# Kernel optimization log

Measured on AMD Instinct MI355X. Metric: run time of the kernel, lower is better.

Reference implementation:

```python
import jax, jax.numpy as jnp
import numpy as np

BN_EPS = 1e-5
NEG_SLOPE = 0.2

def _bn(x, g, b, m, v):
    # inference-mode BatchNorm1d over the channel (last) axis
    return (x - m) * jax.lax.rsqrt(v + BN_EPS) * g + b

def _lrelu(x):
    return jnp.where(x >= 0, x, NEG_SLOPE * x)

def setup_inputs() -> dict:
    key = jax.random.key(0)
    ks = jax.random.split(key, 24)
    B, N, K, Cr, Cin, Cnb, Cout = 2, 65536, 16, 10, 64, 64, 128
    Ccat = Cin + Cnb
    return {
        'xyz': jax.random.normal(ks[0], (B, N, 3), jnp.float32),
        'feature': jax.random.normal(ks[1], (B, N, Cin), jnp.float32),
        'raw_neighbors_feature': jax.random.normal(ks[2], (B, N, K, Cr), jnp.float32),
        'neighbors_idx': jax.random.randint(ks[3], (B, N, K), 0, N, jnp.int32),
        'W_nb': jax.random.normal(ks[4], (Cr, Cnb), jnp.float32) * 0.3,
        'b_nb': jax.random.normal(ks[5], (Cnb,), jnp.float32),
        'g_nb': jax.random.uniform(ks[6], (Cnb,), jnp.float32),
        'be_nb': jax.random.normal(ks[7], (Cnb,), jnp.float32),
        'm_nb': jax.random.normal(ks[8], (Cnb,), jnp.float32),
        'v_nb': jax.random.uniform(ks[9], (Cnb,), jnp.float32),
        'W_attn': jax.random.normal(ks[10], (Ccat, Ccat), jnp.float32) * 0.09,
        'W_out': jax.random.normal(ks[11], (Ccat, Cout), jnp.float32) * 0.09,
        'b_out': jax.random.normal(ks[12], (Cout,), jnp.float32),
        'g_out': jax.random.uniform(ks[13], (Cout,), jnp.float32),
        'be_out': jax.random.normal(ks[14], (Cout,), jnp.float32),
        'm_out': jax.random.normal(ks[15], (Cout,), jnp.float32),
        'v_out': jax.random.uniform(ks[16], (Cout,), jnp.float32),
        'W_sc': jax.random.normal(ks[17], (Cin, Cout), jnp.float32) * 0.12,
        'b_sc': jax.random.normal(ks[18], (Cout,), jnp.float32),
        'g_sc': jax.random.uniform(ks[19], (Cout,), jnp.float32),
        'be_sc': jax.random.normal(ks[20], (Cout,), jnp.float32),
        'm_sc': jax.random.normal(ks[21], (Cout,), jnp.float32),
        'v_sc': jax.random.uniform(ks[22], (Cout,), jnp.float32),
    }

def reference(xyz, feature, raw_neighbors_feature, neighbors_idx,
              W_nb, b_nb, g_nb, be_nb, m_nb, v_nb,
              W_attn,
              W_out, b_out, g_out, be_out, m_out, v_out,
              W_sc, b_sc, g_sc, be_sc, m_sc, v_sc):
    # mlp_neighbor_fea: Linear -> BN1d -> leaky_relu(0.2) over raw neighbor features
    nb = _lrelu(_bn(jnp.einsum('bnkc,cd->bnkd', raw_neighbors_feature, W_nb) + b_nb,
                    g_nb, be_nb, m_nb, v_nb))              # [B,N,K,Cnb]
    # index_points: gather per-point neighbor features [B,N,K,Cin]
    gathered = jax.vmap(lambda f, i: f[i])(feature, neighbors_idx)
    fea = jnp.concatenate([gathered, nb], axis=-1)          # [B,N,K,Ccat]
    # attn pooling: softmax over neighbor axis K of a bias-free linear
    attn = jax.nn.softmax(jnp.einsum('bnkc,cd->bnkd', fea, W_attn), axis=2)
    pooled = jnp.sum(attn * fea, axis=2)                    # [B,N,Ccat]
    out_branch = _bn(pooled @ W_out + b_out, g_out, be_out, m_out, v_out)
    sc_branch = _bn(feature @ W_sc + b_sc, g_sc, be_sc, m_sc, v_sc)
    return _lrelu(sc_branch + out_branch)                   # [B,N,Cout]
```

## Files before the change

kernel.cpp:

```cpp
#include <hip/hip_runtime.h>


#define KNB   16
#define CR    10
#define CIN   64
#define CCAT  128
#define COUT  128
#define NPTS  131072
#define EPS   1e-5f

#define WS_WB   0
#define WS_W3   32768
#define WS_WNB  81920
#define WS_B3   86016
#define WS_BNB  86528

typedef const float* fp;
typedef short bf16x8 __attribute__((ext_vector_type(8)));
typedef float f32x4  __attribute__((ext_vector_type(4)));

__device__ __forceinline__ unsigned short f2bf(float x) {
    unsigned int u = __float_as_uint(x);
    return (unsigned short)((u + 0x7FFFu + ((u >> 16) & 1u)) >> 16);
}
__device__ __forceinline__ unsigned int pack2(float a, float b) {
    return (unsigned int)f2bf(a) | ((unsigned int)f2bf(b) << 16);
}
__device__ __forceinline__ float bf2f(unsigned short h) {
    return __uint_as_float(((unsigned int)h) << 16);
}
__device__ __forceinline__ float lrelu(float x) { return fmaxf(x, 0.2f * x); }

__global__ __launch_bounds__(256) void lfa_prep(
    fp W_nb, fp b_nb, fp g_nb, fp be_nb, fp m_nb, fp v_nb,
    fp W_attn,
    fp W_out, fp b_out, fp g_out, fp be_out, fp m_out, fp v_out,
    fp W_sc,  fp b_sc,  fp g_sc,  fp be_sc,  fp m_sc,  fp v_sc,
    unsigned char* __restrict__ ws)
{
    const int t = blockIdx.x * 256 + threadIdx.x;
    if (t < 2048) {
        const int n0 = t >> 8, s = (t >> 6) & 3, ln = t & 63;
        const int n = (n0 << 4) + (ln & 15);
        unsigned int v[4];
        #pragma unroll
        for (int jj = 0; jj < 4; ++jj) {
            const int k = (s << 5) + ((ln >> 4) << 3) + jj * 2;
            v[jj] = pack2(W_attn[k * CCAT + n], W_attn[(k + 1) * CCAT + n]);
        }
        *(uint4*)(ws + WS_WB + t * 16) = make_uint4(v[0], v[1], v[2], v[3]);
    } else if (t < 5120) {
        const int e = t - 2048;
        const int t8 = e / 384, rem = e % 384, s = rem >> 6, ln = rem & 63;
        const int d = (t8 << 4) + (ln & 15);
        const float so = g_out[d] * rsqrtf(v_out[d] + EPS);
        const float ss = g_sc[d]  * rsqrtf(v_sc[d]  + EPS);
        unsigned int v[4];
        #pragma unroll
        for (int jj = 0; jj < 4; ++jj) {
            float a[2];
            #pragma unroll
            for (int h = 0; h < 2; ++h) {
                const int k = (s << 5) + ((ln >> 4) << 3) + jj * 2 + h;
                a[h] = (k < CCAT) ? W_out[k * COUT + d] * so
                                  : W_sc[(k - CCAT) * COUT + d] * ss;
            }
            v[jj] = pack2(a[0], a[1]);
        }
        *(uint4*)(ws + WS_W3 + e * 16) = make_uint4(v[0], v[1], v[2], v[3]);
    } else if (t < 5376) {
        const int e = t - 5120;
        const int n0 = e >> 6, ln = e & 63;
        const int n = (n0 << 4) + (ln & 15);
        const float sn = g_nb[n] * rsqrtf(v_nb[n] + EPS);
        unsigned int v[4];
        #pragma unroll
        for (int jj = 0; jj < 4; ++jj) {
            float a[2];
            #pragma unroll
            for (int h = 0; h < 2; ++h) {
                const int k = ((ln >> 4) << 3) + jj * 2 + h;
                a[h] = (k < CR) ? W_nb[k * 64 + n] * sn : 0.f;
            }
            v[jj] = pack2(a[0], a[1]);
        }
        *(uint4*)(ws + WS_WNB + e * 16) = make_uint4(v[0], v[1], v[2], v[3]);
    } else if (t < 5504) {
        const int d = t - 5376;
        const float so = g_out[d] * rsqrtf(v_out[d] + EPS);
        const float ss = g_sc[d]  * rsqrtf(v_sc[d]  + EPS);
        ((float*)(ws + WS_B3))[d] =
              (b_out[d] - m_out[d]) * so + be_out[d]
            + (b_sc[d]  - m_sc[d])  * ss + be_sc[d];
    } else if (t < 5568) {
        const int d = t - 5504;
        const float sn = g_nb[d] * rsqrtf(v_nb[d] + EPS);
        ((float*)(ws + WS_BNB))[d] = (b_nb[d] - m_nb[d]) * sn + be_nb[d];
    }
}

__global__ __launch_bounds__(256, 2) void lfa_main(
    fp feature, fp raw, const int* __restrict__ nidx,
    const unsigned char* __restrict__ ws, float* __restrict__ out)
{
    __shared__ __align__(16) unsigned short feaA[4][2][16][136];
    __shared__ __align__(16) unsigned short pooledA[4][16][200];

    const int tid  = threadIdx.x;
    const int w    = tid >> 6;
    const int lane = tid & 63;
    const int quad = lane >> 4;
    const int l15  = lane & 15;
    const int p0   = (blockIdx.x * 4 + w) * 16;
    const int b    = p0 >> 16;

    bf16x8 WB[8][4];
    #pragma unroll
    for (int n0 = 0; n0 < 8; ++n0)
        #pragma unroll
        for (int s = 0; s < 4; ++s)
            WB[n0][s] = *(const bf16x8*)(ws + WS_WB + (((n0 * 4 + s) * 64 + lane) << 4));

    float binb[4];
    #pragma unroll
    for (int j = 0; j < 4; ++j)
        binb[j] = ((const float*)(ws + WS_BNB))[j * 16 + l15];

    #pragma unroll 1
    for (int it = 0; it < 8; ++it) {
        const int pp0 = p0 + it * 2;

        int idxv = 0;
        if (lane < 32) idxv = nidx[pp0 * KNB + lane];

        if (lane < 32) {
            const int pt = lane >> 4, c4 = l15 * 4;
            const float4 cf = *(const float4*)&feature[(size_t)(pp0 + pt) * CIN + c4];
            uint2 pk; pk.x = pack2(cf.x, cf.y); pk.y = pack2(cf.z, cf.w);
            *(uint2*)&pooledA[w][it * 2 + pt][CCAT + c4] = pk;
        }

        #pragma unroll
        for (int pt = 0; pt < 2; ++pt) {
            const int p = pp0 + pt;

            float4 gv[4];
            #pragma unroll
            for (int i = 0; i < 4; ++i) {
                const int ni = __shfl(idxv, pt * 16 + i * 4 + quad, 64);
                gv[i] = *(const float4*)&feature[(size_t)((b << 16) + ni) * CIN + l15 * 4];
            }

            bf16x8 anb = {0, 0, 0, 0, 0, 0, 0, 0};
            {
                const float* rp = raw + (size_t)p * (KNB * CR) + l15 * CR;
                if (quad == 0) {
                    const float2 r0 = *(const float2*)(rp + 0);
                    const float2 r1 = *(const float2*)(rp + 2);
                    const float2 r2 = *(const float2*)(rp + 4);
                    const float2 r3 = *(const float2*)(rp + 6);
                    anb[0] = (short)f2bf(r0.x); anb[1] = (short)f2bf(r0.y);
                    anb[2] = (short)f2bf(r1.x); anb[3] = (short)f2bf(r1.y);
                    anb[4] = (short)f2bf(r2.x); anb[5] = (short)f2bf(r2.y);
                    anb[6] = (short)f2bf(r3.x); anb[7] = (short)f2bf(r3.y);
                } else if (quad == 1) {
                    const float2 r4 = *(const float2*)(rp + 8);
                    anb[0] = (short)f2bf(r4.x); anb[1] = (short)f2bf(r4.y);
                }
            }

            float nbC[4][4];
            #pragma unroll
            for (int n0 = 0; n0 < 4; ++n0) {
                const bf16x8 bw = *(const bf16x8*)(ws + WS_WNB + ((n0 * 64 + lane) << 4));
                f32x4 c = {0.f, 0.f, 0.f, 0.f};
                c = __builtin_amdgcn_mfma_f32_16x16x32_bf16(anb, bw, c, 0, 0, 0);
                #pragma unroll
                for (int r = 0; r < 4; ++r) {
                    const float x = lrelu(c[r] + binb[n0]);
                    nbC[n0][r] = x;
                    feaA[w][pt][quad * 4 + r][64 + n0 * 16 + l15] = f2bf(x);
                }
            }

            #pragma unroll
            for (int i = 0; i < 4; ++i) {
                uint2 pk; pk.x = pack2(gv[i].x, gv[i].y); pk.y = pack2(gv[i].z, gv[i].w);
                *(uint2*)&feaA[w][pt][i * 4 + quad][l15 * 4] = pk;
            }

            bf16x8 A[4];
            #pragma unroll
            for (int s = 0; s < 4; ++s)
                A[s] = *(const bf16x8*)&feaA[w][pt][l15][s * 32 + quad * 8];

            #pragma unroll
            for (int n0 = 0; n0 < 8; ++n0) {
                f32x4 c = {0.f, 0.f, 0.f, 0.f};
                #pragma unroll
                for (int s = 0; s < 4; ++s)
                    c = __builtin_amdgcn_mfma_f32_16x16x32_bf16(A[s], WB[n0][s], c, 0, 0, 0);
                const float e0 = __expf(c[0]), e1 = __expf(c[1]);
                const float e2 = __expf(c[2]), e3 = __expf(c[3]);
                float den = e0 + e1 + e2 + e3;
                float num;
                if (n0 < 4) {
                    num = e0 * bf2f(feaA[w][pt][quad * 4 + 0][n0 * 16 + l15])
                        + e1 * bf2f(feaA[w][pt][quad * 4 + 1][n0 * 16 + l15])
                        + e2 * bf2f(feaA[w][pt][quad * 4 + 2][n0 * 16 + l15])
                        + e3 * bf2f(feaA[w][pt][quad * 4 + 3][n0 * 16 + l15]);
                } else {
                    num = e0 * nbC[n0 - 4][0] + e1 * nbC[n0 - 4][1]
                        + e2 * nbC[n0 - 4][2] + e3 * nbC[n0 - 4][3];
                }
                num += __shfl_xor(num, 16, 64);
                den += __shfl_xor(den, 16, 64);
                num += __shfl_xor(num, 32, 64);
                den += __shfl_xor(den, 32, 64);
                const float pp = __fdividef(num, den);
                if (quad == 0)
                    pooledA[w][it * 2 + pt][n0 * 16 + l15] = f2bf(pp);
            }
        }
    }

    bf16x8 A3[6];
    #pragma unroll
    for (int s = 0; s < 6; ++s)
        A3[s] = *(const bf16x8*)&pooledA[w][l15][s * 32 + quad * 8];
    #pragma unroll
    for (int t = 0; t < 8; ++t) {
        f32x4 c = {0.f, 0.f, 0.f, 0.f};
        #pragma unroll
        for (int s = 0; s < 6; ++s) {
            const bf16x8 bw = *(const bf16x8*)(ws + WS_W3 + (((t * 6 + s) * 64 + lane) << 4));
            c = __builtin_amdgcn_mfma_f32_16x16x32_bf16(A3[s], bw, c, 0, 0, 0);
        }
        const float bz = ((const float*)(ws + WS_B3))[t * 16 + l15];
        #pragma unroll
        for (int r = 0; r < 4; ++r)
            out[(size_t)(p0 + quad * 4 + r) * COUT + t * 16 + l15] = lrelu(c[r] + bz);
    }
}

extern "C" void kernel_launch(void* const* d_in, const int* in_sizes, int n_in,
                              void* d_out, int out_size, void* d_ws, size_t ws_size,
                              hipStream_t stream)
{
    fp feature = (fp)d_in[1];
    fp raw     = (fp)d_in[2];
    const int* nidx = (const int*)d_in[3];
    fp W_nb = (fp)d_in[4],  b_nb = (fp)d_in[5],  g_nb = (fp)d_in[6];
    fp be_nb = (fp)d_in[7], m_nb = (fp)d_in[8],  v_nb = (fp)d_in[9];
    fp W_attn = (fp)d_in[10];
    fp W_out = (fp)d_in[11], b_out = (fp)d_in[12], g_out = (fp)d_in[13];
    fp be_out = (fp)d_in[14], m_out = (fp)d_in[15], v_out = (fp)d_in[16];
    fp W_sc = (fp)d_in[17], b_sc = (fp)d_in[18], g_sc = (fp)d_in[19];
    fp be_sc = (fp)d_in[20], m_sc = (fp)d_in[21], v_sc = (fp)d_in[22];

    hipLaunchKernelGGL(lfa_prep, dim3(22), dim3(256), 0, stream,
                       W_nb, b_nb, g_nb, be_nb, m_nb, v_nb,
                       W_attn,
                       W_out, b_out, g_out, be_out, m_out, v_out,
                       W_sc, b_sc, g_sc, be_sc, m_sc, v_sc,
                       (unsigned char*)d_ws);
    hipLaunchKernelGGL(lfa_main, dim3(2048), dim3(256), 0, stream,
                       feature, raw, nidx,
                       (const unsigned char*)d_ws, (float*)d_out);
}
```

Before: 432.1 us.

## Hoist gathers for both points, shrink LDS staging, raise occupancy, use exp2

Issues the neighbor feature gathers and raw-feature loads for both points of an iteration up front, so their memory latency overlaps. The per-wave LDS tile for fea is halved to a single point buffer and launch bounds request 3 blocks per SM instead of 2. The attention weights are prescaled by log2(e) so the softmax can use the hardware exp2, and bf16 conversion uses the native __bf16 cast. More registers are live at once while the occupancy target is tighter, which risks spills; reusing one fea buffer across both points within a wave relies on in-order execution inside the wave.

```diff
diff --git a/kernel.cpp b/kernel.cpp
--- a/kernel.cpp
+++ b/kernel.cpp
@@ -8,6 +8,7 @@
 #define COUT  128
 #define NPTS  131072
 #define EPS   1e-5f
+#define LOG2E 1.4426950408889634f
 
 #define WS_WB   0
 #define WS_W3   32768
@@ -18,13 +19,14 @@
 typedef const float* fp;
 typedef short bf16x8 __attribute__((ext_vector_type(8)));
 typedef float f32x4  __attribute__((ext_vector_type(4)));
+typedef __bf16 bf16x2 __attribute__((ext_vector_type(2)));
 
 __device__ __forceinline__ unsigned short f2bf(float x) {
-    unsigned int u = __float_as_uint(x);
-    return (unsigned short)((u + 0x7FFFu + ((u >> 16) & 1u)) >> 16);
+    return __builtin_bit_cast(unsigned short, (__bf16)x);
 }
 __device__ __forceinline__ unsigned int pack2(float a, float b) {
-    return (unsigned int)f2bf(a) | ((unsigned int)f2bf(b) << 16);
+    bf16x2 v; v.x = (__bf16)a; v.y = (__bf16)b;
+    return __builtin_bit_cast(unsigned int, v);
 }
 __device__ __forceinline__ float bf2f(unsigned short h) {
     return __uint_as_float(((unsigned int)h) << 16);
@@ -46,7 +48,8 @@
         #pragma unroll
         for (int jj = 0; jj < 4; ++jj) {
             const int k = (s << 5) + ((ln >> 4) << 3) + jj * 2;
-            v[jj] = pack2(W_attn[k * CCAT + n], W_attn[(k + 1) * CCAT + n]);
+            v[jj] = pack2(W_attn[k * CCAT + n] * LOG2E,
+                          W_attn[(k + 1) * CCAT + n] * LOG2E);
         }
         *(uint4*)(ws + WS_WB + t * 16) = make_uint4(v[0], v[1], v[2], v[3]);
     } else if (t < 5120) {
@@ -99,11 +102,11 @@
     }
 }
 
-__global__ __launch_bounds__(256, 2) void lfa_main(
+__global__ __launch_bounds__(256, 3) void lfa_main(
     fp feature, fp raw, const int* __restrict__ nidx,
     const unsigned char* __restrict__ ws, float* __restrict__ out)
 {
-    __shared__ __align__(16) unsigned short feaA[4][2][16][136];
+    __shared__ __align__(16) unsigned short feaA[4][16][136];
     __shared__ __align__(16) unsigned short pooledA[4][16][200];
 
     const int tid  = threadIdx.x;
@@ -140,59 +143,64 @@
             *(uint2*)&pooledA[w][it * 2 + pt][CCAT + c4] = pk;
         }
 
-        #pragma unroll
-        for (int pt = 0; pt < 2; ++pt) {
-            const int p = pp0 + pt;
-
-            float4 gv[4];
+        float4 gv[2][4];
+        #pragma unroll
+        for (int pt = 0; pt < 2; ++pt)
             #pragma unroll
             for (int i = 0; i < 4; ++i) {
                 const int ni = __shfl(idxv, pt * 16 + i * 4 + quad, 64);
-                gv[i] = *(const float4*)&feature[(size_t)((b << 16) + ni) * CIN + l15 * 4];
-            }
-
-            bf16x8 anb = {0, 0, 0, 0, 0, 0, 0, 0};
-            {
-                const float* rp = raw + (size_t)p * (KNB * CR) + l15 * CR;
-                if (quad == 0) {
-                    const float2 r0 = *(const float2*)(rp + 0);
-                    const float2 r1 = *(const float2*)(rp + 2);
-                    const float2 r2 = *(const float2*)(rp + 4);
-                    const float2 r3 = *(const float2*)(rp + 6);
-                    anb[0] = (short)f2bf(r0.x); anb[1] = (short)f2bf(r0.y);
-                    anb[2] = (short)f2bf(r1.x); anb[3] = (short)f2bf(r1.y);
-                    anb[4] = (short)f2bf(r2.x); anb[5] = (short)f2bf(r2.y);
-                    anb[6] = (short)f2bf(r3.x); anb[7] = (short)f2bf(r3.y);
-                } else if (quad == 1) {
-                    const float2 r4 = *(const float2*)(rp + 8);
-                    anb[0] = (short)f2bf(r4.x); anb[1] = (short)f2bf(r4.y);
-                }
-            }
+                gv[pt][i] = *(const float4*)&feature[(size_t)((b << 16) + ni) * CIN + l15 * 4];
+            }
+
+        bf16x8 anb[2];
+        #pragma unroll
+        for (int pt = 0; pt < 2; ++pt) {
+            bf16x8 a = {0, 0, 0, 0, 0, 0, 0, 0};
+            const float* rp = raw + (size_t)(pp0 + pt) * (KNB * CR) + l15 * CR;
+            if (quad == 0) {
+                const float2 r0 = *(const float2*)(rp + 0);
+                const float2 r1 = *(const float2*)(rp + 2);
+                const float2 r2 = *(const float2*)(rp + 4);
+                const float2 r3 = *(const float2*)(rp + 6);
+                a[0] = (short)f2bf(r0.x); a[1] = (short)f2bf(r0.y);
+                a[2] = (short)f2bf(r1.x); a[3] = (short)f2bf(r1.y);
+                a[4] = (short)f2bf(r2.x); a[5] = (short)f2bf(r2.y);
+                a[6] = (short)f2bf(r3.x); a[7] = (short)f2bf(r3.y);
+            } else if (quad == 1) {
+                const float2 r4 = *(const float2*)(rp + 8);
+                a[0] = (short)f2bf(r4.x); a[1] = (short)f2bf(r4.y);
+            }
+            anb[pt] = a;
+        }
+
+        #pragma unroll
+        for (int pt = 0; pt < 2; ++pt) {
 
             float nbC[4][4];
             #pragma unroll
             for (int n0 = 0; n0 < 4; ++n0) {
                 const bf16x8 bw = *(const bf16x8*)(ws + WS_WNB + ((n0 * 64 + lane) << 4));
                 f32x4 c = {0.f, 0.f, 0.f, 0.f};
-                c = __builtin_amdgcn_mfma_f32_16x16x32_bf16(anb, bw, c, 0, 0, 0);
+                c = __builtin_amdgcn_mfma_f32_16x16x32_bf16(anb[pt], bw, c, 0, 0, 0);
                 #pragma unroll
                 for (int r = 0; r < 4; ++r) {
                     const float x = lrelu(c[r] + binb[n0]);
                     nbC[n0][r] = x;
-                    feaA[w][pt][quad * 4 + r][64 + n0 * 16 + l15] = f2bf(x);
+                    feaA[w][quad * 4 + r][64 + n0 * 16 + l15] = f2bf(x);
                 }
             }
 
             #pragma unroll
             for (int i = 0; i < 4; ++i) {
-                uint2 pk; pk.x = pack2(gv[i].x, gv[i].y); pk.y = pack2(gv[i].z, gv[i].w);
-                *(uint2*)&feaA[w][pt][i * 4 + quad][l15 * 4] = pk;
+                uint2 pk; pk.x = pack2(gv[pt][i].x, gv[pt][i].y);
+                pk.y = pack2(gv[pt][i].z, gv[pt][i].w);
+                *(uint2*)&feaA[w][i * 4 + quad][l15 * 4] = pk;
             }
 
             bf16x8 A[4];
             #pragma unroll
             for (int s = 0; s < 4; ++s)
-                A[s] = *(const bf16x8*)&feaA[w][pt][l15][s * 32 + quad * 8];
+                A[s] = *(const bf16x8*)&feaA[w][l15][s * 32 + quad * 8];
 
             #pragma unroll
             for (int n0 = 0; n0 < 8; ++n0) {
@@ -200,15 +208,17 @@
                 #pragma unroll
                 for (int s = 0; s < 4; ++s)
                     c = __builtin_amdgcn_mfma_f32_16x16x32_bf16(A[s], WB[n0][s], c, 0, 0, 0);
-                const float e0 = __expf(c[0]), e1 = __expf(c[1]);
-                const float e2 = __expf(c[2]), e3 = __expf(c[3]);
+                const float e0 = __builtin_amdgcn_exp2f(c[0]);
+                const float e1 = __builtin_amdgcn_exp2f(c[1]);
+                const float e2 = __builtin_amdgcn_exp2f(c[2]);
+                const float e3 = __builtin_amdgcn_exp2f(c[3]);
                 float den = e0 + e1 + e2 + e3;
                 float num;
                 if (n0 < 4) {
-                    num = e0 * bf2f(feaA[w][pt][quad * 4 + 0][n0 * 16 + l15])
-                        + e1 * bf2f(feaA[w][pt][quad * 4 + 1][n0 * 16 + l15])
-                        + e2 * bf2f(feaA[w][pt][quad * 4 + 2][n0 * 16 + l15])
-                        + e3 * bf2f(feaA[w][pt][quad * 4 + 3][n0 * 16 + l15]);
+                    num = e0 * bf2f(feaA[w][quad * 4 + 0][n0 * 16 + l15])
+                        + e1 * bf2f(feaA[w][quad * 4 + 1][n0 * 16 + l15])
+                        + e2 * bf2f(feaA[w][quad * 4 + 2][n0 * 16 + l15])
+                        + e3 * bf2f(feaA[w][quad * 4 + 3][n0 * 16 + l15]);
                 } else {
                     num = e0 * nbC[n0 - 4][0] + e1 * nbC[n0 - 4][1]
                         + e2 * nbC[n0 - 4][2] + e3 * nbC[n0 - 4][3];
```

After: 655.4 us. +51.7%, slower.
